# Performance work log

Measured on AMD Instinct MI355X. Metric: run time of the kernel, lower is better.

## Reference

```python
import jax, jax.numpy as jnp
import numpy as np

VOCAB = 1000
HID = 512      # hidden_size == context_size (hidden is initialized to context)
EMB = 512


def setup_inputs() -> dict:
    key = jax.random.key(0)
    ks = jax.random.split(key, 8)
    B = 128
    scale_ih = 1.0 / np.sqrt(HID)
    inp = {
        "context": jax.random.normal(ks[0], (B, HID), dtype=jnp.float32),
        "embed_table": jax.random.normal(ks[1], (VOCAB, EMB), dtype=jnp.float32) * 0.02,
        "W_ih": jax.random.uniform(ks[2], (4 * HID, HID + EMB), minval=-scale_ih, maxval=scale_ih, dtype=jnp.float32),
        "b_ih": jax.random.uniform(ks[3], (4 * HID,), minval=-scale_ih, maxval=scale_ih, dtype=jnp.float32),
        "W_hh": jax.random.uniform(ks[4], (4 * HID, HID), minval=-scale_ih, maxval=scale_ih, dtype=jnp.float32),
        "b_hh": jax.random.uniform(ks[5], (4 * HID,), minval=-scale_ih, maxval=scale_ih, dtype=jnp.float32),
        "W_out": jax.random.uniform(ks[6], (VOCAB, HID), minval=-scale_ih, maxval=scale_ih, dtype=jnp.float32),
        "b_out": jax.random.uniform(ks[7], (VOCAB,), minval=-scale_ih, maxval=scale_ih, dtype=jnp.float32),
        "start_id": 1,
        "max_seq_len": 256,
    }
    return inp


def reference(context, embed_table, W_ih, b_ih, W_hh, b_hh, W_out, b_out, start_id, max_seq_len):
    B = context.shape[0]
    hidden0 = context                                   # torch: hidden = context
    cell0 = jnp.zeros((B, HID), dtype=context.dtype)
    init_emb = jnp.broadcast_to(embed_table[start_id], (B, EMB))

    def step(carry, _):
        h, c, emb = carry
        x = jnp.concatenate([context, emb], axis=1)     # [B, C+E]
        gates = x @ W_ih.T + b_ih + h @ W_hh.T + b_hh   # [B, 4H]
        i_g, f_g, g_g, o_g = jnp.split(gates, 4, axis=1)  # torch LSTMCell gate order
        i_g = jax.nn.sigmoid(i_g)
        f_g = jax.nn.sigmoid(f_g)
        g_g = jnp.tanh(g_g)
        o_g = jax.nn.sigmoid(o_g)
        c_new = f_g * c + i_g * g_g
        h_new = o_g * jnp.tanh(c_new)
        out = h_new @ W_out.T + b_out                   # [B, V]
        next_emb = embed_table[jnp.argmax(out, axis=1)]  # greedy-decode feedback
        return (h_new, c_new, next_emb), out

    (h_f, c_f, _), outs = jax.lax.scan(step, (hidden0, cell0, init_emb), None, length=max_seq_len)
    output_tensor = jnp.transpose(outs, (1, 0, 2))      # [B, T, V]
    return output_tensor, h_f, c_f
```

## Files before the change

### kernel.cpp

```cpp
#include <hip/hip_runtime.h>
#include <float.h>
#include <math.h>

#define B_    128
#define H_    512
#define V_    1000
#define T_    256
#define G4_   2048
#define NBLK  256
#define SPIN_MAX (1 << 17)

#define AT_LOAD(p)    __hip_atomic_load((p), __ATOMIC_RELAXED, __HIP_MEMORY_SCOPE_AGENT)
#define AT_STORE(p,v) __hip_atomic_store((p), (v), __ATOMIC_RELAXED, __HIP_MEMORY_SCOPE_AGENT)

#define PIN4(v_) asm volatile("" : "+v"((v_).x), "+v"((v_).y), "+v"((v_).z), "+v"((v_).w))

__device__ __forceinline__ float dot4(float4 a, float4 b, float acc) {
  return fmaf(a.x, b.x, fmaf(a.y, b.y, fmaf(a.z, b.z, fmaf(a.w, b.w, acc))));
}

__device__ __forceinline__ float red16(float x) {
  x += __int_as_float(__builtin_amdgcn_mov_dpp(__float_as_int(x), 0xB1,  0xF, 0xF, true));
  x += __int_as_float(__builtin_amdgcn_mov_dpp(__float_as_int(x), 0x4E,  0xF, 0xF, true));
  x += __int_as_float(__builtin_amdgcn_mov_dpp(__float_as_int(x), 0x141, 0xF, 0xF, true));
  x += __int_as_float(__builtin_amdgcn_mov_dpp(__float_as_int(x), 0x140, 0xF, 0xF, true));
  return x;
}

__global__ __launch_bounds__(256) void gemm_nt_k512(
    const float* __restrict__ A, int M,
    const float* __restrict__ Bm, int ldb, int koff,
    const float* __restrict__ bias1, const float* __restrict__ bias2,
    float* __restrict__ C, int ldc, int ileave)
{
  __shared__ float As[16][68];
  __shared__ float Bs[16][68];
  const int tid = threadIdx.x;
  const int m0 = blockIdx.y * 64, n0 = blockIdx.x * 64;
  const int tm = tid & 15, tn = tid >> 4;
  const int lm = tid & 63, kq = tid >> 6;
  float acc[4][4] = {};
  for (int k0 = 0; k0 < 512; k0 += 16) {
    float4 av = make_float4(0.f, 0.f, 0.f, 0.f);
    if (m0 + lm < M) av = *(const float4*)(A + (size_t)(m0 + lm) * 512 + k0 + kq * 4);
    float4 bv = *(const float4*)(Bm + (size_t)(n0 + lm) * ldb + koff + k0 + kq * 4);
    __syncthreads();
    As[kq*4+0][lm] = av.x; As[kq*4+1][lm] = av.y; As[kq*4+2][lm] = av.z; As[kq*4+3][lm] = av.w;
    Bs[kq*4+0][lm] = bv.x; Bs[kq*4+1][lm] = bv.y; Bs[kq*4+2][lm] = bv.z; Bs[kq*4+3][lm] = bv.w;
    __syncthreads();
#pragma unroll
    for (int kk = 0; kk < 16; ++kk) {
      const float4 a = *(const float4*)&As[kk][tm * 4];
      const float4 b = *(const float4*)&Bs[kk][tn * 4];
      const float aa[4] = {a.x, a.y, a.z, a.w};
      const float bb[4] = {b.x, b.y, b.z, b.w};
#pragma unroll
      for (int i = 0; i < 4; ++i)
#pragma unroll
        for (int j = 0; j < 4; ++j)
          acc[i][j] = fmaf(aa[i], bb[j], acc[i][j]);
    }
  }
#pragma unroll
  for (int i = 0; i < 4; ++i) {
    const int m = m0 + tm * 4 + i;
    if (m < M) {
#pragma unroll
      for (int j = 0; j < 4; ++j) {
        const int n = n0 + tn * 4 + j;
        float v = acc[i][j];
        if (bias1) v += bias1[n];
        if (bias2) v += bias2[n];
        const size_t idx = ileave ? ((size_t)m * ldc + (size_t)(n & 511) * 4 + (n >> 9))
                                  : ((size_t)m * ldc + n);
        C[idx] = v;
      }
    }
  }
}

__global__ __launch_bounds__(256) void init_kernel(
    const float* __restrict__ ctx, float* __restrict__ hbuf,
    unsigned long long* __restrict__ amax,
    int* __restrict__ hdone, const int* __restrict__ start_id)
{
  const int i = blockIdx.x * blockDim.x + threadIdx.x;
  ((float4*)(hbuf + B_ * H_))[i] = ((const float4*)ctx)[i];
  if (i < B_ * 32) {
    const int m = i & 31;
    const unsigned long long w = (m == 0)
        ? ((((unsigned long long)__float_as_uint(FLT_MAX)) << 32) |
           (1u << 16) | (unsigned)(*start_id))
        : ((((unsigned long long)__float_as_uint(-FLT_MAX)) << 32) | (1u << 16));
    amax[(size_t)B_ * 32 + i] = w;
  }
  if (i < 2 * 8 * 32) hdone[i * 16] = 0;
}

__global__ __launch_bounds__(512, 2) void decoder_main(
    const float* __restrict__ Whh,
    const float* __restrict__ Wout,
    const float* __restrict__ bout,
    const float* __restrict__ proj,
    const float* __restrict__ basep,
    float* __restrict__ hbuf,
    unsigned long long* __restrict__ amax,
    int* __restrict__ hdone,
    float* __restrict__ out)
{
  __shared__ struct alignas(16) SM {
    float hs[16][640];
    float gbase[16][68];
    float gbuf2[2][16][68];
    float lbuf2[2][16][34];
    float sbout[32];
    int   tok[16];
  } sm;

  const int tid  = threadIdx.x;
  const int bid  = blockIdx.x;
  const int gid  = bid >> 5;
  const int mem  = bid & 31;
  const int lane = tid & 63;
  const int w    = tid >> 6;
  const int row_base = gid * 16;
  const int vb   = mem * 32;

  const int q1  = lane >> 4;
  const int kc  = lane & 15;
  const int blk = w & 3;
  const int par = w >> 2;
  const int hoff  = par * 256 + kc * 16;
  const int hcol  = (par * 16 + kc) * 20;

  float4 w1r[4][4];
#pragma unroll
  for (int i = 0; i < 4; ++i) {
    const float* p = Whh + (size_t)(blk * 512 + mem * 16 + q1 * 4 + i) * H_ + hoff;
#pragma unroll
    for (int j = 0; j < 4; ++j) w1r[i][j] = *(const float4*)(p + j * 4);
  }
  const int v0 = vb + blk * 8 + q1 * 2;
  float4 w2r[2][4];
#pragma unroll
  for (int jj = 0; jj < 2; ++jj) {
    const int vv = (v0 + jj < V_) ? (v0 + jj) : (V_ - 1);
    const float* p = Wout + (size_t)vv * H_ + hoff;
#pragma unroll
    for (int j = 0; j < 4; ++j) w2r[jj][j] = *(const float4*)(p + j * 4);
  }
#pragma unroll
  for (int i = 0; i < 4; ++i) {
    PIN4(w1r[i][0]); PIN4(w1r[i][1]); PIN4(w1r[i][2]); PIN4(w1r[i][3]);
  }
#pragma unroll
  for (int jj = 0; jj < 2; ++jj) {
    PIN4(w2r[jj][0]); PIN4(w2r[jj][1]); PIN4(w2r[jj][2]); PIN4(w2r[jj][3]);
  }

#pragma unroll
  for (int kx = 0; kx < 2; ++kx) {
    const int e = tid + kx * 512;
    const int r = e >> 6, c = e & 63;
    sm.gbase[r][c] = basep[(size_t)(row_base + r) * G4_ + mem * 64 + c];
  }
  if (tid < 32) sm.sbout[tid] = (vb + tid < V_) ? bout[vb + tid] : 0.f;

  float c_reg = 0.f;
  const size_t BTVo = (size_t)B_ * T_ * V_;

  {
    const unsigned long long* hq =
        (const unsigned long long*)(hbuf + (size_t)B_ * H_ + (size_t)row_base * H_);
    unsigned long long v[8];
#pragma unroll
    for (int i = 0; i < 8; ++i) v[i] = AT_LOAD(&hq[tid + i * 512]);
#pragma unroll
    for (int i = 0; i < 8; ++i) {
      const int idx = tid + i * 512;
      const int row = idx >> 8, cp = idx & 255;
      *(unsigned long long*)&sm.hs[row][(cp >> 3) * 20 + (cp & 7) * 2] = v[i];
    }
  }
  __syncthreads();

  for (int t = 0; t < T_; ++t) {
    float* hdst = hbuf + (size_t)(t & 1) * (B_ * H_);

#pragma unroll 1
    for (int r = 0; r < 16; ++r) {
      const float* hr = &sm.hs[r][hcol];
      const float4 h0 = *(const float4*)(hr + 0);
      const float4 h1 = *(const float4*)(hr + 4);
      const float4 h2 = *(const float4*)(hr + 8);
      const float4 h3 = *(const float4*)(hr + 12);
      float a0 = dot4(w1r[0][3], h3, dot4(w1r[0][2], h2, dot4(w1r[0][1], h1, dot4(w1r[0][0], h0, 0.f))));
      float a1 = dot4(w1r[1][3], h3, dot4(w1r[1][2], h2, dot4(w1r[1][1], h1, dot4(w1r[1][0], h0, 0.f))));
      float a2 = dot4(w1r[2][3], h3, dot4(w1r[2][2], h2, dot4(w1r[2][1], h1, dot4(w1r[2][0], h0, 0.f))));
      float a3 = dot4(w1r[3][3], h3, dot4(w1r[3][2], h2, dot4(w1r[3][1], h1, dot4(w1r[3][0], h0, 0.f))));
      a0 = red16(a0); a1 = red16(a1); a2 = red16(a2); a3 = red16(a3);
      if (kc < 4) {
        const float av = (kc == 0) ? a0 : (kc == 1) ? a1 : (kc == 2) ? a2 : a3;
        sm.gbuf2[par][r][(q1 * 4 + kc) * 4 + blk] = av;
      }
    }

    {
      const int prow = tid >> 5, pj = tid & 31;
      const unsigned expect = (unsigned)(t + 1) << 16;
      const unsigned long long* ap =
          amax + ((size_t)((t + 1) & 1) * B_ + row_base + prow) * 32;
      unsigned long long wv = AT_LOAD(&ap[pj]);
      for (int it = 0; (((unsigned)wv ^ expect) & 0xFFFF0000u) && it < SPIN_MAX; ++it) {
        __builtin_amdgcn_s_sleep(1);
        wv = AT_LOAD(&ap[pj]);
      }
      __atomic_signal_fence(__ATOMIC_ACQ_REL);
      float v  = __uint_as_float((unsigned)(wv >> 32));
      int   ix = (int)((unsigned)wv & 0xFFFFu);
#pragma unroll
      for (int d = 16; d >= 1; d >>= 1) {
        const float vo = __shfl_xor(v, d, 32);
        const int   io = __shfl_xor(ix, d, 32);
        if (vo > v || (vo == v && io < ix)) { v = vo; ix = io; }
      }
      if (pj == 0) sm.tok[prow] = (ix >= 0 && ix < V_) ? ix : 0;
    }
    __syncthreads();

    if (tid < 256) {
      const int rl = tid >> 4, ul = tid & 15;
      const int tk = sm.tok[rl];
      const float4 ga = *(const float4*)&sm.gbuf2[0][rl][ul * 4];
      const float4 gb = *(const float4*)&sm.gbuf2[1][rl][ul * 4];
      const float4 gc = *(const float4*)&sm.gbase[rl][ul * 4];
      const float4 gp = *(const float4*)&proj[(size_t)tk * G4_ + (size_t)(mem * 16 + ul) * 4];
      const float gx = ga.x + gb.x + gc.x + gp.x;
      const float gy = ga.y + gb.y + gc.y + gp.y;
      const float gz = ga.z + gb.z + gc.z + gp.z;
      const float gw = ga.w + gb.w + gc.w + gp.w;
      const float ig = 1.f / (1.f + expf(-gx));
      const float fg = 1.f / (1.f + expf(-gy));
      const float gg = tanhf(gz);
      const float og = 1.f / (1.f + expf(-gw));
      const float cn = fg * c_reg + ig * gg;
      c_reg = cn;
      const float hn = og * tanhf(cn);
      const int row = row_base + rl, hid = mem * 16 + ul;
      const float hn2 = __shfl_down(hn, 1);
      if ((ul & 1) == 0) {
        const unsigned long long pk =
            (unsigned long long)__float_as_uint(hn) |
            (((unsigned long long)__float_as_uint(hn2)) << 32);
        AT_STORE((unsigned long long*)&hdst[(size_t)row * H_ + hid], pk);
      }
      if (t == T_ - 1) {
        out[BTVo + (size_t)row * H_ + hid] = hn;
        out[BTVo + (size_t)B_ * H_ + (size_t)row * H_ + hid] = cn;
      }
    }
    __syncthreads();
    if (tid == 0)
      AT_STORE(&hdone[(((t & 1) * 8 + gid) * 32 + mem) * 16], t + 2);

    if (tid < 32) {
      int* fp = &hdone[(((t & 1) * 8 + gid) * 32 + tid) * 16];
      for (int it = 0; AT_LOAD(fp) != t + 2 && it < SPIN_MAX; ++it)
        __builtin_amdgcn_s_sleep(1);
    }
    __atomic_signal_fence(__ATOMIC_ACQ_REL);
    __syncthreads();

    {
      const unsigned long long* hq =
          (const unsigned long long*)(hdst + (size_t)row_base * H_);
      unsigned long long v[8];
#pragma unroll
      for (int i = 0; i < 8; ++i) v[i] = AT_LOAD(&hq[tid + i * 512]);
#pragma unroll
      for (int i = 0; i < 8; ++i) {
        const int idx = tid + i * 512;
        const int row = idx >> 8, cp = idx & 255;
        *(unsigned long long*)&sm.hs[row][(cp >> 3) * 20 + (cp & 7) * 2] = v[i];
      }
    }
    __syncthreads();

#pragma unroll 1
    for (int r = 0; r < 16; ++r) {
      const float* hr = &sm.hs[r][hcol];
      const float4 h0 = *(const float4*)(hr + 0);
      const float4 h1 = *(const float4*)(hr + 4);
      const float4 h2 = *(const float4*)(hr + 8);
      const float4 h3 = *(const float4*)(hr + 12);
      float b0 = dot4(w2r[0][3], h3, dot4(w2r[0][2], h2, dot4(w2r[0][1], h1, dot4(w2r[0][0], h0, 0.f))));
      float b1 = dot4(w2r[1][3], h3, dot4(w2r[1][2], h2, dot4(w2r[1][1], h1, dot4(w2r[1][0], h0, 0.f))));
      b0 = red16(b0); b1 = red16(b1);
      if (kc < 2)
        sm.lbuf2[par][r][blk * 8 + q1 * 2 + kc] = (kc == 0) ? b0 : b1;
    }
    __syncthreads();

    {
      const int r = tid >> 5, j = tid & 31;
      float v = sm.lbuf2[0][r][j] + sm.lbuf2[1][r][j] + sm.sbout[j];
      if (vb + j < V_)
        out[((size_t)(row_base + r) * T_ + t) * V_ + vb + j] = v;
      else
        v = -FLT_MAX;
      int ix = j;
#pragma unroll
      for (int d = 16; d >= 1; d >>= 1) {
        const float vo = __shfl_xor(v, d, 32);
        const int   io = __shfl_xor(ix, d, 32);
        if (vo > v || (vo == v && io < ix)) { v = vo; ix = io; }
      }
      if (j == 0) {
        const unsigned long long pk =
            (((unsigned long long)__float_as_uint(v)) << 32) |
            ((unsigned)(t + 2) << 16) | (unsigned)(vb + ix);
        AT_STORE(&amax[((size_t)(t & 1) * B_ + row_base + r) * 32 + mem], pk);
      }
    }
  }
}

extern "C" void kernel_launch(void* const* d_in, const int* in_sizes, int n_in,
                              void* d_out, int out_size, void* d_ws, size_t ws_size,
                              hipStream_t stream)
{
  const float* ctx   = (const float*)d_in[0];
  const float* emb   = (const float*)d_in[1];
  const float* Wih   = (const float*)d_in[2];
  const float* bih   = (const float*)d_in[3];
  const float* Whh   = (const float*)d_in[4];
  const float* bhh   = (const float*)d_in[5];
  const float* Wout  = (const float*)d_in[6];
  const float* bout  = (const float*)d_in[7];
  const int*   start = (const int*)d_in[8];
  float* out = (float*)d_out;

  char* ws = (char*)d_ws;
  float* proj  = (float*)(ws + 0);
  float* basep = (float*)(ws + 8192000);
  float* hbuf  = (float*)(ws + 9240576);
  unsigned long long* amax = (unsigned long long*)(ws + 9764864);
  int*   hdone = (int*)(ws + 9830400);

  hipLaunchKernelGGL(gemm_nt_k512, dim3(32, 2), dim3(256), 0, stream,
                     ctx, B_, Wih, 1024, 0, bih, bhh, basep, G4_, 1);
  hipLaunchKernelGGL(gemm_nt_k512, dim3(32, 16), dim3(256), 0, stream,
                     emb, V_, Wih, 1024, 512, (const float*)nullptr, (const float*)nullptr,
                     proj, G4_, 1);
  hipLaunchKernelGGL(init_kernel, dim3(64), dim3(256), 0, stream,
                     ctx, hbuf, amax, hdone, start);

  void* args[] = {(void*)&Whh, (void*)&Wout, (void*)&bout, (void*)&proj, (void*)&basep,
                  (void*)&hbuf, (void*)&amax, (void*)&hdone, (void*)&out};
  hipLaunchCooperativeKernel(reinterpret_cast<const void*>(decoder_main),
                             dim3(NBLK), dim3(512), args, 0, stream);
}
```

Measured before the change: 3.078 ms.

## Double decoder block size to 1024 threads splitting K four ways, use fast exp activations

Expands each persistent decoder block from 512 to 1024 threads, splitting the K dimension of both the recurrent and output matvecs four ways instead of two. Each thread now holds half as many register-resident weights and does half the FMAs per row, with partial sums combined through larger shared buffers. Sigmoid and tanh are switched to __expf-based approximations. The aim is to shorten the per-step serial latency, at the cost of larger reductions, fewer threads active in the gate and argmax phases, and slightly lower activation accuracy.

After: 3.247 ms. 1.05x slower.

```diff
diff --git a/kernel.cpp b/kernel.cpp
--- a/kernel.cpp
+++ b/kernel.cpp
@@ -25,6 +25,14 @@
   x += __int_as_float(__builtin_amdgcn_mov_dpp(__float_as_int(x), 0x141, 0xF, 0xF, true));
   x += __int_as_float(__builtin_amdgcn_mov_dpp(__float_as_int(x), 0x140, 0xF, 0xF, true));
   return x;
+}
+
+__device__ __forceinline__ float fsigmoid(float x) {
+  return 1.f / (1.f + __expf(-x));
+}
+__device__ __forceinline__ float ftanh(float x) {
+  const float e = __expf(2.f * fabsf(x));
+  return copysignf(1.f - 2.f / (e + 1.f), x);
 }
 
 __global__ __launch_bounds__(256) void gemm_nt_k512(
@@ -97,7 +105,7 @@
   if (i < 2 * 8 * 32) hdone[i * 16] = 0;
 }
 
-__global__ __launch_bounds__(512, 2) void decoder_main(
+__global__ __launch_bounds__(1024) void decoder_main(
     const float* __restrict__ Whh,
     const float* __restrict__ Wout,
     const float* __restrict__ bout,
@@ -111,8 +119,8 @@
   __shared__ struct alignas(16) SM {
     float hs[16][640];
     float gbase[16][68];
-    float gbuf2[2][16][68];
-    float lbuf2[2][16][34];
+    float gbuf4[4][16][68];
+    float lbuf4[4][16][34];
     float sbout[32];
     int   tok[16];
   } sm;
@@ -126,42 +134,36 @@
   const int row_base = gid * 16;
   const int vb   = mem * 32;
 
-  const int q1  = lane >> 4;
-  const int kc  = lane & 15;
-  const int blk = w & 3;
-  const int par = w >> 2;
-  const int hoff  = par * 256 + kc * 16;
-  const int hcol  = (par * 16 + kc) * 20;
-
-  float4 w1r[4][4];
+  const int q1   = lane >> 4;
+  const int kc   = lane & 15;
+  const int blk  = w & 3;
+  const int par2 = w >> 2;
+  const int hoff = par2 * 128 + kc * 8;
+  const int hcol = (par2 * 8 + (kc >> 1)) * 20 + (kc & 1) * 8;
+
+  float4 w1r[4][2];
 #pragma unroll
   for (int i = 0; i < 4; ++i) {
     const float* p = Whh + (size_t)(blk * 512 + mem * 16 + q1 * 4 + i) * H_ + hoff;
-#pragma unroll
-    for (int j = 0; j < 4; ++j) w1r[i][j] = *(const float4*)(p + j * 4);
+    w1r[i][0] = *(const float4*)(p);
+    w1r[i][1] = *(const float4*)(p + 4);
   }
   const int v0 = vb + blk * 8 + q1 * 2;
-  float4 w2r[2][4];
+  float4 w2r[2][2];
 #pragma unroll
   for (int jj = 0; jj < 2; ++jj) {
     const int vv = (v0 + jj < V_) ? (v0 + jj) : (V_ - 1);
     const float* p = Wout + (size_t)vv * H_ + hoff;
-#pragma unroll
-    for (int j = 0; j < 4; ++j) w2r[jj][j] = *(const float4*)(p + j * 4);
-  }
-#pragma unroll
-  for (int i = 0; i < 4; ++i) {
-    PIN4(w1r[i][0]); PIN4(w1r[i][1]); PIN4(w1r[i][2]); PIN4(w1r[i][3]);
-  }
-#pragma unroll
-  for (int jj = 0; jj < 2; ++jj) {
-    PIN4(w2r[jj][0]); PIN4(w2r[jj][1]); PIN4(w2r[jj][2]); PIN4(w2r[jj][3]);
-  }
-
-#pragma unroll
-  for (int kx = 0; kx < 2; ++kx) {
-    const int e = tid + kx * 512;
-    const int r = e >> 6, c = e & 63;
+    w2r[jj][0] = *(const float4*)(p);
+    w2r[jj][1] = *(const float4*)(p + 4);
+  }
+#pragma unroll
+  for (int i = 0; i < 4; ++i) { PIN4(w1r[i][0]); PIN4(w1r[i][1]); }
+#pragma unroll
+  for (int jj = 0; jj < 2; ++jj) { PIN4(w2r[jj][0]); PIN4(w2r[jj][1]); }
+
+  {
+    const int r = tid >> 6, c = tid & 63;
     sm.gbase[r][c] = basep[(size_t)(row_base + r) * G4_ + mem * 64 + c];
   }
   if (tid < 32) sm.sbout[tid] = (vb + tid < V_) ? bout[vb + tid] : 0.f;
@@ -172,12 +174,12 @@
   {
     const unsigned long long* hq =
         (const unsigned long long*)(hbuf + (size_t)B_ * H_ + (size_t)row_base * H_);
-    unsigned long long v[8];
-#pragma unroll
-    for (int i = 0; i < 8; ++i) v[i] = AT_LOAD(&hq[tid + i * 512]);
-#pragma unroll
-    for (int i = 0; i < 8; ++i) {
-      const int idx = tid + i * 512;
+    unsigned long long v[4];
+#pragma unroll
+    for (int i = 0; i < 4; ++i) v[i] = AT_LOAD(&hq[tid + i * 1024]);
+#pragma unroll
+    for (int i = 0; i < 4; ++i) {
+      const int idx = tid + i * 1024;
       const int row = idx >> 8, cp = idx & 255;
       *(unsigned long long*)&sm.hs[row][(cp >> 3) * 20 + (cp & 7) * 2] = v[i];
     }
@@ -192,20 +194,18 @@
       const float* hr = &sm.hs[r][hcol];
       const float4 h0 = *(const float4*)(hr + 0);
       const float4 h1 = *(const float4*)(hr + 4);
-      const float4 h2 = *(const float4*)(hr + 8);
-      const float4 h3 = *(const float4*)(hr + 12);
-      float a0 = dot4(w1r[0][3], h3, dot4(w1r[0][2], h2, dot4(w1r[0][1], h1, dot4(w1r[0][0], h0, 0.f))));
-      float a1 = dot4(w1r[1][3], h3, dot4(w1r[1][2], h2, dot4(w1r[1][1], h1, dot4(w1r[1][0], h0, 0.f))));
-      float a2 = dot4(w1r[2][3], h3, dot4(w1r[2][2], h2, dot4(w1r[2][1], h1, dot4(w1r[2][0], h0, 0.f))));
-      float a3 = dot4(w1r[3][3], h3, dot4(w1r[3][2], h2, dot4(w1r[3][1], h1, dot4(w1r[3][0], h0, 0.f))));
+      float a0 = dot4(w1r[0][1], h1, dot4(w1r[0][0], h0, 0.f));
+      float a1 = dot4(w1r[1][1], h1, dot4(w1r[1][0], h0, 0.f));
+      float a2 = dot4(w1r[2][1], h1, dot4(w1r[2][0], h0, 0.f));
+      float a3 = dot4(w1r[3][1], h1, dot4(w1r[3][0], h0, 0.f));
       a0 = red16(a0); a1 = red16(a1); a2 = red16(a2); a3 = red16(a3);
       if (kc < 4) {
         const float av = (kc == 0) ? a0 : (kc == 1) ? a1 : (kc == 2) ? a2 : a3;
-        sm.gbuf2[par][r][(q1 * 4 + kc) * 4 + blk] = av;
-      }
-    }
-
-    {
+        sm.gbuf4[par2][r][(q1 * 4 + kc) * 4 + blk] = av;
+      }
+    }
+
+    if (tid < 512) {
       const int prow = tid >> 5, pj = tid & 31;
       const unsigned expect = (unsigned)(t + 1) << 16;
       const unsigned long long* ap =
@@ -231,21 +231,23 @@
     if (tid < 256) {
       const int rl = tid >> 4, ul = tid & 15;
       const int tk = sm.tok[rl];
-      const float4 ga = *(const float4*)&sm.gbuf2[0][rl][ul * 4];
-      const float4 gb = *(const float4*)&sm.gbuf2[1][rl][ul * 4];
+      const float4 g0 = *(const float4*)&sm.gbuf4[0][rl][ul * 4];
+      const float4 g1 = *(const float4*)&sm.gbuf4[1][rl][ul * 4];
+      const float4 g2 = *(const float4*)&sm.gbuf4[2][rl][ul * 4];
+      const float4 g3 = *(const float4*)&sm.gbuf4[3][rl][ul * 4];
       const float4 gc = *(const float4*)&sm.gbase[rl][ul * 4];
       const float4 gp = *(const float4*)&proj[(size_t)tk * G4_ + (size_t)(mem * 16 + ul) * 4];
-      const float gx = ga.x + gb.x + gc.x + gp.x;
-      const float gy = ga.y + gb.y + gc.y + gp.y;
-      const float gz = ga.z + gb.z + gc.z + gp.z;
-      const float gw = ga.w + gb.w + gc.w + gp.w;
-      const float ig = 1.f / (1.f + expf(-gx));
-      const float fg = 1.f / (1.f + expf(-gy));
-      const float gg = tanhf(gz);
-      const float og = 1.f / (1.f + expf(-gw));
+      const float gx = (g0.x + g1.x) + (g2.x + g3.x) + gc.x + gp.x;
+      const float gy = (g0.y + g1.y) + (g2.y + g3.y) + gc.y + gp.y;
+      const float gz = (g0.z + g1.z) + (g2.z + g3.z) + gc.z + gp.z;
+      const float gw = (g0.w + g1.w) + (g2.w + g3.w) + gc.w + gp.w;
+      const float ig = fsigmoid(gx);
+      const float fg = fsigmoid(gy);
+      const float gg = ftanh(gz);
+      const float og = fsigmoid(gw);
       const float cn = fg * c_reg + ig * gg;
       c_reg = cn;
-      const float hn = og * tanhf(cn);
+      const float hn = og * ftanh(cn);
       const int row = row_base + rl, hid = mem * 16 + ul;
       const float hn2 = __shfl_down(hn, 1);
       if ((ul & 1) == 0) {
@@ -274,12 +276,12 @@
     {
       const unsigned long long* hq =
           (const unsigned long long*)(hdst + (size_t)row_base * H_);
-      unsigned long long v[8];
-#pragma unroll
-      for (int i = 0; i < 8; ++i) v[i] = AT_LOAD(&hq[tid + i * 512]);
-#pragma unroll
-      for (int i = 0; i < 8; ++i) {
-        const int idx = tid + i * 512;
+      unsigned long long v[4];
+#pragma unroll
+      for (int i = 0; i < 4; ++i) v[i] = AT_LOAD(&hq[tid + i * 1024]);
+#pragma unroll
+      for (int i = 0; i < 4; ++i) {
+        const int idx = tid + i * 1024;
         const int row = idx >> 8, cp = idx & 255;
         *(unsigned long long*)&sm.hs[row][(cp >> 3) * 20 + (cp & 7) * 2] = v[i];
       }
@@ -291,19 +293,18 @@
       const float* hr = &sm.hs[r][hcol];
       const float4 h0 = *(const float4*)(hr + 0);
       const float4 h1 = *(const float4*)(hr + 4);
-      const float4 h2 = *(const float4*)(hr + 8);
-      const float4 h3 = *(const float4*)(hr + 12);
-      float b0 = dot4(w2r[0][3], h3, dot4(w2r[0][2], h2, dot4(w2r[0][1], h1, dot4(w2r[0][0], h0, 0.f))));
-      float b1 = dot4(w2r[1][3], h3, dot4(w2r[1][2], h2, dot4(w2r[1][1], h1, dot4(w2r[1][0], h0, 0.f))));
+      float b0 = dot4(w2r[0][1], h1, dot4(w2r[0][0], h0, 0.f));
+      float b1 = dot4(w2r[1][1], h1, dot4(w2r[1][0], h0, 0.f));
       b0 = red16(b0); b1 = red16(b1);
       if (kc < 2)
-        sm.lbuf2[par][r][blk * 8 + q1 * 2 + kc] = (kc == 0) ? b0 : b1;
-    }
-    __syncthreads();
-
-    {
+        sm.lbuf4[par2][r][blk * 8 + q1 * 2 + kc] = (kc == 0) ? b0 : b1;
+    }
+    __syncthreads();
+
+    if (tid < 512) {
       const int r = tid >> 5, j = tid & 31;
-      float v = sm.lbuf2[0][r][j] + sm.lbuf2[1][r][j] + sm.sbout[j];
+      float v = (sm.lbuf4[0][r][j] + sm.lbuf4[1][r][j]) +
+                (sm.lbuf4[2][r][j] + sm.lbuf4[3][r][j]) + sm.sbout[j];
       if (vb + j < V_)
         out[((size_t)(row_base + r) * T_ + t) * V_ + vb + j] = v;
       else
@@ -358,5 +359,5 @@
   void* args[] = {(void*)&Whh, (void*)&Wout, (void*)&bout, (void*)&proj, (void*)&basep,
                   (void*)&hbuf, (void*)&amax, (void*)&hdone, (void*)&out};
   hipLaunchCooperativeKernel(reinterpret_cast<const void*>(decoder_main),
-                             dim3(NBLK), dim3(512), args, 0, stream);
-}
+                             dim3(NBLK), dim3(1024), args, 0, stream);
+}
```
